# Kernel tuning notes

Hardware: AMD Instinct MI355X
Metric: run time of the kernel (lower is better)

The kernel has to match this reference:

```python
import jax, jax.numpy as jnp
import numpy as np
from math import factorial

R_MAX = 3.5
BASIS = 20
NORM2MOM_SILU = 1.679177  # e3nn normalize2mom constant for silu

# ---------- Wigner 3j (e3nn convention: real basis, Frobenius norm 1) ----------

def _su2_cg(j1, m1, j2, m2, j3, m3):
    if m3 != m1 + m2:
        return 0.0
    vmin = int(max(-j1 + j2 + m3, -j1 + m1, 0))
    vmax = int(min(j2 + j3 + m1, j3 - j1 + j2, j3 + m3))
    f = lambda n: factorial(round(n))
    C = ((2 * j3 + 1) * f(j3 + j1 - j2) * f(j3 - j1 + j2) * f(j1 + j2 - j3)
         * f(j3 + m3) * f(j3 - m3)
         / (f(j1 + j2 + j3 + 1) * f(j1 - m1) * f(j1 + m1) * f(j2 - m2) * f(j2 + m2))) ** 0.5
    S = 0.0
    for v in range(vmin, vmax + 1):
        S += (-1.0) ** (v + j2 + m2) / f(v) * f(j2 + j3 + m1 - v) * f(j1 - m1 + v) \
             / f(j3 - j1 + j2 - v) / f(j3 + m3 - v) / f(v + j1 - j2 - m3)
    return C * S


def _real_basis(l):
    q = np.zeros((2 * l + 1, 2 * l + 1), dtype=np.complex128)
    for m in range(-l, 0):
        q[l + m, l + abs(m)] = 2 ** -0.5
        q[l + m, l - abs(m)] = -1j * 2 ** -0.5
    q[l, l] = 1.0
    for m in range(1, l + 1):
        q[l + m, l + abs(m)] = (-1) ** m * 2 ** -0.5
        q[l + m, l - abs(m)] = 1j * (-1) ** m * 2 ** -0.5
    return (-1j) ** l * q


def wigner_3j(l1, l2, l3):
    C = np.zeros((2 * l1 + 1, 2 * l2 + 1, 2 * l3 + 1))
    for m1 in range(-l1, l1 + 1):
        for m2 in range(-l2, l2 + 1):
            if abs(m1 + m2) <= l3:
                C[l1 + m1, l2 + m2, l3 + m1 + m2] = _su2_cg(l1, m1, l2, m2, l3, m1 + m2)
    Q1, Q2, Q3 = _real_basis(l1), _real_basis(l2), _real_basis(l3)
    Cr = np.einsum('ij,kl,mn,ikn->jlm', Q1, Q2, np.conj(Q3.T), C.astype(np.complex128))
    assert np.abs(Cr.imag).max() < 1e-4
    Cr = Cr.real
    return (Cr / np.linalg.norm(Cr)).astype(np.float32)

# tp2 paths: (l1 from middle, l2 from sh) -> 2e (even parity, triangle inequality)
TP2_PATHS = [(0, 2), (1, 1), (1, 3), (2, 0), (2, 2), (3, 1), (3, 3)]
W3J = {p: jnp.asarray(wigner_3j(p[0], p[1], 2)) for p in TP2_PATHS}
ALPHA2 = (5.0 / 35.0) ** 0.5  # component norm: sqrt(dim(2e) / fan_in), fan_in = 7 paths * mul 5

# ---------- spherical harmonics, lmax=3, component normalization (e3nn axis convention) ----------

def spherical_harmonics(v):  # v: [E,3] unit vectors -> [E,16]
    x, y, z = v[:, 0], v[:, 1], v[:, 2]
    x2, y2, z2 = x * x, y * y, z * z
    s3, s5, s15 = 3.0 ** 0.5, 5.0 ** 0.5, 15.0 ** 0.5
    s70_4, s105, s42_4 = 70.0 ** 0.5 / 4, 105.0 ** 0.5, 42.0 ** 0.5 / 4
    s7_2, s105_2 = 7.0 ** 0.5 / 2, 105.0 ** 0.5 / 2
    sh = [jnp.ones_like(x),
          s3 * x, s3 * y, s3 * z,
          s15 * x * z, s15 * x * y, s5 * (y2 - 0.5 * (x2 + z2)), s15 * y * z, 0.5 * s15 * (z2 - x2),
          s70_4 * x * (3 * z2 - x2), s105 * x * y * z, s42_4 * x * (5 * y2 - 1.0),
          s7_2 * y * (5 * y2 - 3.0), s42_4 * z * (5 * y2 - 1.0), s105_2 * y * (z2 - x2),
          s70_4 * z * (z2 - 3 * x2)]
    return jnp.stack(sh, axis=-1)


def soft_one_hot(d):  # smooth_finite basis with cutoff on [0, R_MAX]
    values = jnp.linspace(0.0, R_MAX, BASIS + 2)[1:-1]
    step = R_MAX / (BASIS + 1)
    diff = (d[:, None] - values) / step
    def u(t):
        ts = jnp.where(t > 0, t, 1.0)
        return jnp.where(t > 0, jnp.exp(-1.0 / ts), 0.0)
    return 1.14136 * np.e ** 2 * u(diff + 1.0) * u(1.0 - diff)


def setup_inputs() -> dict:
    key = jax.random.key(0)
    ks = jax.random.split(key, 7)
    N, E = 50000, 600000
    edge_from = jax.random.randint(ks[2], (E,), 0, N)
    # no self-loops (avoids zero-length edge vectors, as radius_graph would)
    edge_to = (edge_from + jax.random.randint(ks[3], (E,), 1, N)) % N
    return {
        'x': jax.random.normal(ks[0], (N, 1), jnp.float32),
        'pos': jax.random.normal(ks[1], (N, 3), jnp.float32),
        'edge_from': edge_from,
        'edge_to': edge_to,
        'W1': jax.random.normal(ks[4], (20, 30), jnp.float32),
        'W2': jax.random.normal(ks[5], (30, 20), jnp.float32),
        'tp2_w': jax.random.normal(ks[6], (7, 5), jnp.float32),
    }


def reference(x, pos, edge_from, edge_to, W1, W2, tp2_w):
    E = edge_from.shape[0]
    N = x.shape[0]
    num_neighbors = 6.0
    edge_vec = pos[edge_to] - pos[edge_from]                 # [E,3]
    dist = jnp.linalg.norm(edge_vec, axis=1)                 # [E]
    sh = spherical_harmonics(edge_vec / dist[:, None])       # [E,16]
    emb = soft_one_hot(dist)                                 # [E,20]
    # FullyConnectedNet([20,30,20], silu) with e3nn normalization
    h = NORM2MOM_SILU * jax.nn.silu(emb @ W1 / jnp.sqrt(20.0))
    tp_w = (h @ W2 / jnp.sqrt(30.0)).reshape(E, 4, 5)        # per-edge tp1 weights
    s = x[edge_to, 0]                                        # [E] gathered 0e scalars
    sh_blocks = [sh[:, 0:1], sh[:, 1:4], sh[:, 4:9], sh[:, 9:16]]
    # tp1: 0e x l -> l ; alpha * w3j(0,l,l) collapses to identity per l
    mid = jnp.concatenate([
        (s[:, None, None] * tp_w[:, l, :, None] * sh_blocks[l][:, None, :]).reshape(E, 5 * (2 * l + 1))
        for l in range(4)], axis=-1)                         # [E,80]
    node_mid = jax.ops.segment_sum(mid, edge_from, num_segments=N) / jnp.sqrt(num_neighbors)
    m = node_mid[edge_to]                                    # [E,80]
    offs = [0, 5, 20, 45, 80]
    mid_blocks = [m[:, offs[l]:offs[l + 1]].reshape(E, 5, 2 * l + 1) for l in range(4)]
    out_e = jnp.zeros((E, 5), dtype=x.dtype)
    for p, (l1, l2) in enumerate(TP2_PATHS):
        out_e = out_e + ALPHA2 * jnp.einsum('ijk,eui,ej,u->ek', W3J[(l1, l2)],
                                            mid_blocks[l1], sh_blocks[l2], tp2_w[p])
    node_out = jax.ops.segment_sum(out_e, edge_from, num_segments=N) / jnp.sqrt(num_neighbors)
    Co = jnp.argmax(jnp.bincount(edge_to, length=N))         # torch.mode -> most frequent target node
    return node_out[Co]                                      # [5] = 1x2e
```

## Files before the change

kernel.cpp:

```cpp
#include <hip/hip_runtime.h>
#include <cmath>
#include <complex>
#include <algorithm>

#define NBH   16
#define CAP_S 512
#define CAP_T 64
#define CAP_M 4096
#define EB    64
#define HW_MAX 12544
#define BM_MAX 1568

namespace w3jhost {
static double fact(int n){
  static const double f[13]={1,1,2,6,24,120,720,5040,40320,362880,3628800,39916800,479001600};
  return f[n];
}
static double su2_cg(int j1,int m1,int j2,int m2,int j3,int m3){
  if(m3!=m1+m2) return 0.0;
  int vmin = std::max(std::max(-j1+j2+m3,-j1+m1),0);
  int vmax = std::min(std::min(j2+j3+m1, j3-j1+j2), j3+m3);
  double C = std::sqrt((double)(2*j3+1)*fact(j3+j1-j2)*fact(j3-j1+j2)*fact(j1+j2-j3)*fact(j3+m3)*fact(j3-m3)
            /(fact(j1+j2+j3+1)*fact(j1-m1)*fact(j1+m1)*fact(j2-m2)*fact(j2+m2)));
  double S=0.0;
  for(int v=vmin;v<=vmax;v++){
    double sgn = ((v+j2+m2)&1)?-1.0:1.0;
    S += sgn/fact(v)*fact(j2+j3+m1-v)*fact(j1-m1+v)/fact(j3-j1+j2-v)/fact(j3+m3-v)/fact(v+j1-j2-m3);
  }
  return C*S;
}
static void real_basis(int l, std::complex<double> q[7][7]){
  for(int i=0;i<7;i++)for(int j=0;j<7;j++) q[i][j]=0.0;
  const double r = std::sqrt(0.5);
  for(int m=-l;m<0;m++){ q[l+m][l-m]=r; q[l+m][l+m]=std::complex<double>(0.0,-r); }
  q[l][l]=1.0;
  for(int m=1;m<=l;m++){ double sg=(m&1)?-1.0:1.0; q[l+m][l+m]=sg*r; q[l+m][l-m]=std::complex<double>(0.0,sg*r); }
  std::complex<double> f;
  switch(l&3){ case 0: f={1,0};break; case 1: f={0,-1};break; case 2: f={-1,0};break; default: f={0,1};break; }
  for(int i=0;i<7;i++)for(int j=0;j<7;j++) q[i][j]*=f;
}
}

struct W3JArg { float w[675]; };

static W3JArg compute_w3j(){
  using namespace w3jhost;
  W3JArg out{};
  const int pl1[7]={0,1,1,2,2,3,3}, pl2[7]={2,1,3,0,2,1,3};
  int off=0;
  for(int p=0;p<7;p++){
    int l1=pl1[p], l2=pl2[p], l3=2;
    int n1=2*l1+1, n2=2*l2+1, n3=2*l3+1;
    double C[7][7][5];
    for(int i=0;i<7;i++)for(int k=0;k<7;k++)for(int n=0;n<5;n++) C[i][k][n]=0.0;
    for(int m1=-l1;m1<=l1;m1++)for(int m2=-l2;m2<=l2;m2++)
      if(std::abs(m1+m2)<=l3) C[l1+m1][l2+m2][l3+m1+m2]=su2_cg(l1,m1,l2,m2,l3,m1+m2);
    std::complex<double> Q1[7][7],Q2[7][7],Q3[7][7];
    real_basis(l1,Q1); real_basis(l2,Q2); real_basis(l3,Q3);
    double Cr[7][7][5]; double nrm=0.0;
    for(int a=0;a<n1;a++)for(int b=0;b<n2;b++)for(int c=0;c<n3;c++){
      std::complex<double> s(0.0,0.0);
      for(int i=0;i<n1;i++)for(int k=0;k<n2;k++)for(int n=0;n<n3;n++){
        double cv=C[i][k][n]; if(cv==0.0) continue;
        s += Q1[i][a]*Q2[k][b]*std::conj(Q3[n][c])*cv;
      }
      Cr[a][b][c]=s.real(); nrm+=s.real()*s.real();
    }
    nrm=std::sqrt(nrm);
    for(int a=0;a<n1;a++)for(int b=0;b<n2;b++)for(int c=0;c<n3;c++)
      out.w[off+(a*n2+b)*n3+c]=(float)(Cr[a][b][c]/nrm);
    off+=n1*n2*n3;
  }
  return out;
}
static const W3JArg g_w3j = compute_w3j();

__device__ __forceinline__ void calc_sh(float x,float y,float z,float* sh){
  float x2=x*x,y2=y*y,z2=z*z;
  const float s3=1.7320508075688772f, s5=2.2360679774997896f, s15=3.872983346207417f;
  const float s70_4=2.091650066335189f, s105=10.246950765959598f, s42_4=1.6201851746019651f;
  const float s7_2=1.3228756555322954f, s105_2=5.123475382979799f;
  sh[0]=1.f;
  sh[1]=s3*x; sh[2]=s3*y; sh[3]=s3*z;
  sh[4]=s15*x*z; sh[5]=s15*x*y; sh[6]=s5*(y2-0.5f*(x2+z2)); sh[7]=s15*y*z; sh[8]=0.5f*s15*(z2-x2);
  sh[9]=s70_4*x*(3.f*z2-x2); sh[10]=s105*x*y*z; sh[11]=s42_4*x*(5.f*y2-1.f);
  sh[12]=s7_2*y*(5.f*y2-3.f); sh[13]=s42_4*z*(5.f*y2-1.f); sh[14]=s105_2*y*(z2-x2); sh[15]=s70_4*z*(z2-3.f*x2);
}

__global__ void __launch_bounds__(1024,1)
k_hist(const int* __restrict__ eto, int E, int N, int* __restrict__ histg){
  __shared__ int hist[HW_MAX];
  const int HW=(N+3)>>2;
  const int tid=threadIdx.x;
  for(int w=tid;w<HW;w+=1024) hist[w]=0;
  __syncthreads();
  int nQ=(E+3)>>2;
  for(int q=blockIdx.x*1024+tid;q<nQ;q+=NBH*1024){
    int e=q*4;
    if(e+3<E){
      int4 v=*reinterpret_cast<const int4*>(eto+e);
      atomicAdd(&hist[v.x>>2], 1<<((v.x&3)*8));
      atomicAdd(&hist[v.y>>2], 1<<((v.y&3)*8));
      atomicAdd(&hist[v.z>>2], 1<<((v.z&3)*8));
      atomicAdd(&hist[v.w>>2], 1<<((v.w&3)*8));
    } else {
      for(;e<E;e++){ int t=eto[e]; atomicAdd(&hist[t>>2], 1<<((t&3)*8)); }
    }
  }
  __syncthreads();
  for(int w=tid;w<HW;w+=1024) histg[blockIdx.x*HW+w]=hist[w];
}

__global__ void __launch_bounds__(256,1)
k_argmax(const int* __restrict__ histg, int N, unsigned long long* __restrict__ packed){
  const int HW=(N+3)>>2;
  int w=blockIdx.x*256+threadIdx.x;
  unsigned long long lm=0ull;
  if(w<HW){
    int c0=0,c1=0,c2=0,c3=0;
    #pragma unroll
    for(int b=0;b<NBH;b++){
      int h=histg[b*HW+w];
      c0+=h&255; c1+=(h>>8)&255; c2+=(h>>16)&255; c3+=(int)((unsigned)h>>24);
    }
    int node=w*4;
    if(c0>0)          lm=max(lm,(((unsigned long long)(unsigned)c0)<<32)|(unsigned long long)(0xFFFFFFFFu-(unsigned)(node  )));
    if(node+1<N&&c1>0)lm=max(lm,(((unsigned long long)(unsigned)c1)<<32)|(unsigned long long)(0xFFFFFFFFu-(unsigned)(node+1)));
    if(node+2<N&&c2>0)lm=max(lm,(((unsigned long long)(unsigned)c2)<<32)|(unsigned long long)(0xFFFFFFFFu-(unsigned)(node+2)));
    if(node+3<N&&c3>0)lm=max(lm,(((unsigned long long)(unsigned)c3)<<32)|(unsigned long long)(0xFFFFFFFFu-(unsigned)(node+3)));
  }
  #pragma unroll
  for(int off=32;off;off>>=1){
    unsigned long long o=__shfl_xor(lm,off);
    lm=max(lm,o);
  }
  if((threadIdx.x&63)==0 && lm) atomicMax(packed,lm);
}

__global__ void __launch_bounds__(256,1)
k_collect(const int* __restrict__ efrom, int E,
          const unsigned long long* __restrict__ packed,
          int* __restrict__ S, int* __restrict__ numS){
  int co=(int)(0xFFFFFFFFu-(unsigned)((*packed)&0xFFFFFFFFull));
  int q=blockIdx.x*256+threadIdx.x;
  int e=q*4;
  if(e+3<E){
    int4 v=*reinterpret_cast<const int4*>(efrom+e);
    int f[4]={v.x,v.y,v.z,v.w};
    #pragma unroll
    for(int k=0;k<4;k++){
      if(f[k]==co){
        int p=atomicAdd(numS,1);
        if(p<CAP_S) S[p]=e+k;
      }
    }
  } else {
    for(;e<E;e++){
      if(efrom[e]==co){
        int p=atomicAdd(numS,1);
        if(p<CAP_S) S[p]=e;
      }
    }
  }
}

__global__ void __launch_bounds__(256,1)
k_scanM(const int* __restrict__ efrom, const int* __restrict__ eto, int E, int N,
        const int* __restrict__ S, const int* __restrict__ numS,
        int* __restrict__ M, int* __restrict__ numM){
  __shared__ int bitmap[BM_MAX];
  __shared__ int Te[CAP_T];
  __shared__ int Tlist[CAP_T];
  __shared__ int nTs;
  const int tid=threadIdx.x;
  int ns=*numS; if(ns>CAP_S) ns=CAP_S;
  int nsc=min(ns,CAP_T);
  const int BMW=(N+31)>>5;
  for(int w=tid;w<BMW;w+=256) bitmap[w]=0;
  if(tid<nsc) Te[tid]=eto[S[tid]];
  __syncthreads();
  if(tid<64){
    bool keep=false; int myv=0;
    if(tid<nsc){
      myv=Te[tid];
      keep=true;
      for(int k=0;k<tid;k++) if(Te[k]==myv){ keep=false; break; }
    }
    unsigned long long mask=__ballot(keep);
    if(keep){
      int slot=__popcll(mask&((1ull<<tid)-1ull));
      Tlist[slot]=myv;
    }
    if(tid==0) nTs=__popcll(mask);
  }
  __syncthreads();
  int nT=nTs;
  if(tid<nT){ int v=Tlist[tid]; atomicOr(&bitmap[v>>5], 1<<(v&31)); }
  __syncthreads();
  int q=blockIdx.x*256+tid;
  int e=q*4;
  if(e+3<E){
    int4 v=*reinterpret_cast<const int4*>(efrom+e);
    int f[4]={v.x,v.y,v.z,v.w};
    #pragma unroll
    for(int k=0;k<4;k++){
      int s=f[k];
      if((bitmap[s>>5]>>(s&31))&1){
        int sl=0;
        for(int kk=0;kk<nT;kk++) if(Tlist[kk]==s){ sl=kk; break; }
        int p=atomicAdd(numM,1);
        if(p<CAP_M) M[p]=(e+k)|(sl<<20);
      }
    }
  } else {
    for(;e<E;e++){
      int s=efrom[e];
      if((bitmap[s>>5]>>(s&31))&1){
        int sl=0;
        for(int kk=0;kk<nT;kk++) if(Tlist[kk]==s){ sl=kk; break; }
        int p=atomicAdd(numM,1);
        if(p<CAP_M) M[p]=e|(sl<<20);
      }
    }
  }
}

__global__ void __launch_bounds__(1024,1)
k_mlp(const float* __restrict__ x, const float* __restrict__ pos,
      const int* __restrict__ efrom, const int* __restrict__ eto,
      const float* __restrict__ W1, const float* __restrict__ W2,
      const int* __restrict__ M, const int* __restrict__ numM,
      float* __restrict__ nmid_g){
  __shared__ float W1s[600], W2s[600];
  __shared__ float shs[EB*16], embs[EB*20], hs[EB*30], tws[EB*20];
  __shared__ float es_[EB], dd_[EB];
  __shared__ int   sl_[EB];
  const int tid=threadIdx.x;
  int nm=*numM; if(nm>CAP_M) nm=CAP_M;
  for(int i=tid;i<600;i+=1024){ W1s[i]=W1[i]; W2s[i]=W2[i]; }
  int nb=(int)gridDim.x;
  int per=(nm+nb-1)/nb;
  int lo=min(nm,(int)blockIdx.x*per), hi=min(nm,lo+per);
  for(int base=lo;base<hi;base+=EB){
    int cnt=min(EB,hi-base);
    __syncthreads();
    if(tid<cnt){
      int m=M[base+tid];
      int e=m&0xFFFFF, sl=m>>20;
      sl_[tid]=sl;
      int a=efrom[e], b=eto[e];
      float dx=pos[3*b]-pos[3*a], dy=pos[3*b+1]-pos[3*a+1], dz=pos[3*b+2]-pos[3*a+2];
      float d=sqrtf(dx*dx+dy*dy+dz*dz);
      float inv=1.f/d;
      calc_sh(dx*inv,dy*inv,dz*inv,&shs[tid*16]);
      dd_[tid]=d;
      es_[tid]=x[b]*(0.18257418583505536f*0.4082482904638631f);
    }
    __syncthreads();
    for(int t=tid;t<cnt*20;t+=1024){
      int ee=t/20, i=t-ee*20;
      const float inv_step=21.f/3.5f;
      const float pref=(float)(1.14136*7.3890560989306495);
      float di=dd_[ee]*inv_step;
      float A=di-(float)i, B=(float)(i+2)-di;
      float ua=(A>0.f)?expf(-1.f/A):0.f;
      float ub=(B>0.f)?expf(-1.f/B):0.f;
      embs[ee*20+i]=pref*ua*ub;
    }
    __syncthreads();
    for(int t=tid;t<cnt*30;t+=1024){
      int ee=t/30, j=t-ee*30;
      float z=0.f;
      #pragma unroll
      for(int i=0;i<20;i++) z+=embs[ee*20+i]*W1s[i*30+j];
      z*=0.22360679774997896f;
      hs[ee*30+j]=1.679177f*z/(1.f+expf(-z));
    }
    __syncthreads();
    for(int t=tid;t<cnt*20;t+=1024){
      int ee=t/20, c=t-ee*20;
      float v=0.f;
      #pragma unroll
      for(int j=0;j<30;j++) v+=hs[ee*30+j]*W2s[j*20+c];
      tws[ee*20+c]=v;
    }
    __syncthreads();
    for(int t=tid;t<cnt*80;t+=1024){
      int ee=t/80, oo=t-ee*80;
      int sl=sl_[ee];
      int l,u,mm;
      if(oo<5){ l=0; u=oo; mm=0; }
      else if(oo<20){ int r=oo-5;  l=1; u=r/3; mm=r-u*3; }
      else if(oo<45){ int r=oo-20; l=2; u=r/5; mm=r-u*5; }
      else          { int r=oo-45; l=3; u=r/7; mm=r-u*7; }
      float val=es_[ee]*tws[ee*20+l*5+u]*shs[ee*16+l*l+mm];
      atomicAdd(&nmid_g[sl*80+oo],val);
    }
  }
}

__global__ void __launch_bounds__(1024,1)
k_final(const float* __restrict__ pos, const int* __restrict__ efrom, const int* __restrict__ eto,
        const float* __restrict__ tp2, const int* __restrict__ S, const int* __restrict__ numS,
        const float* __restrict__ nmid_g, W3JArg w3, float* __restrict__ out5){
  __shared__ float w3s[675];
  __shared__ float nmid_s[CAP_T*80];
  __shared__ float shs[EB*16];
  __shared__ float tp2s[35];
  __shared__ float acc[5];
  __shared__ int   Te[CAP_T], Tlist[CAP_T], sl_[EB], nTs;
  const int tid=threadIdx.x;
  for(int i=tid;i<675;i+=1024) w3s[i]=w3.w[i];
  if(tid<35) tp2s[tid]=tp2[tid];
  if(tid<5) acc[tid]=0.f;
  int ns=*numS; if(ns>CAP_S) ns=CAP_S;
  int nsc=min(ns,CAP_T);
  if(tid<nsc) Te[tid]=eto[S[tid]];
  __syncthreads();
  if(tid<64){
    bool keep=false; int myv=0;
    if(tid<nsc){
      myv=Te[tid];
      keep=true;
      for(int k=0;k<tid;k++) if(Te[k]==myv){ keep=false; break; }
    }
    unsigned long long mask=__ballot(keep);
    if(keep){
      int slot=__popcll(mask&((1ull<<tid)-1ull));
      Tlist[slot]=myv;
    }
    if(tid==0) nTs=__popcll(mask);
  }
  __syncthreads();
  int nT=nTs;
  for(int i=tid;i<nT*80;i+=1024) nmid_s[i]=nmid_g[i];
  for(int base=0;base<ns;base+=EB){
    int cnt=min(EB,ns-base);
    __syncthreads();
    if(tid<cnt){
      int e=S[base+tid];
      int a=efrom[e], b=eto[e];
      int sl=-1;
      for(int k=0;k<nT;k++) if(Tlist[k]==b){ sl=k; break; }
      sl_[tid]=sl;
      if(sl>=0){
        float dx=pos[3*b]-pos[3*a], dy=pos[3*b+1]-pos[3*a+1], dz=pos[3*b+2]-pos[3*a+2];
        float d=sqrtf(dx*dx+dy*dy+dz*dz);
        float inv=1.f/d;
        calc_sh(dx*inv,dy*inv,dz*inv,&shs[tid*16]);
      }
    }
    __syncthreads();
    for(int t=tid;t<cnt*35;t+=1024){
      int ee=t/35, r=t-ee*35, p=r/5, u=r-p*5;
      int sl=sl_[ee];
      if(sl>=0){
        int l1=(p+1)>>1;
        int l2=(0x3636>>(2*p))&3;
        const unsigned long long wbpack=
          (25ULL<<9)|(70ULL<<18)|(175ULL<<27)|(200ULL<<36)|(325ULL<<45)|(430ULL<<54);
        int wb=(int)((wbpack>>(9*p))&511ULL);
        int n1=2*l1+1, n2=2*l2+1;
        float tu=tp2s[p*5+u];
        float o0=0.f,o1=0.f,o2=0.f,o3=0.f,o4=0.f;
        const float* mrow=&nmid_s[sl*80+5*l1*l1+u*n1];
        const float* shrow=&shs[ee*16+l2*l2];
        const float* Wp=&w3s[wb];
        for(int i=0;i<n1;i++){
          float mi=mrow[i]*tu;
          for(int j=0;j<n2;j++){
            float c=mi*shrow[j];
            const float* Wk=Wp+(i*n2+j)*5;
            o0+=Wk[0]*c; o1+=Wk[1]*c; o2+=Wk[2]*c; o3+=Wk[3]*c; o4+=Wk[4]*c;
          }
        }
        atomicAdd(&acc[0],o0); atomicAdd(&acc[1],o1); atomicAdd(&acc[2],o2);
        atomicAdd(&acc[3],o3); atomicAdd(&acc[4],o4);
      }
    }
    __syncthreads();
  }
  __syncthreads();
  const float scale=0.37796447300922725f*0.4082482904638631f;
  if(tid<5) out5[tid]=acc[tid]*scale;
}

extern "C" void kernel_launch(void* const* d_in, const int* in_sizes, int n_in,
                              void* d_out, int out_size, void* d_ws, size_t ws_size,
                              hipStream_t stream){
  const float* x    =(const float*)d_in[0];
  const float* pos  =(const float*)d_in[1];
  const int*   efrom=(const int*)  d_in[2];
  const int*   eto  =(const int*)  d_in[3];
  const float* W1   =(const float*)d_in[4];
  const float* W2   =(const float*)d_in[5];
  const float* tp2  =(const float*)d_in[6];
  int N=in_sizes[0], E=in_sizes[2];
  int HW=(N+3)>>2;

  char* ws=(char*)d_ws;
  size_t o=0;
  unsigned long long* packed=(unsigned long long*)(ws+o); o+=8;
  int* numS=(int*)(ws+o);                   o+=4;
  int* numM=(int*)(ws+o);                   o+=4;
  o=(o+63)&~(size_t)63;
  float* nmid_g=(float*)(ws+o);             o+=(size_t)CAP_T*80*4;
  size_t zlen=o;
  int* histg=(int*)(ws+o);                  o+=(size_t)NBH*HW*4;
  int* S=(int*)(ws+o);                      o+=(size_t)CAP_S*4;
  int* M=(int*)(ws+o);                      o+=(size_t)CAP_M*4;

  (void)hipMemsetAsync(d_ws,0,zlen,stream);

  int nQ=(E+3)>>2;
  int gScan=(nQ+255)/256;
  int gArg =(HW+255)/256;
  k_hist   <<<NBH,1024,0,stream>>>(eto,E,N,histg);
  k_argmax <<<gArg,256,0,stream>>>(histg,N,packed);
  k_collect<<<gScan,256,0,stream>>>(efrom,E,packed,S,numS);
  k_scanM  <<<gScan,256,0,stream>>>(efrom,eto,E,N,S,numS,M,numM);
  k_mlp    <<<16,1024,0,stream>>>(x,pos,efrom,eto,W1,W2,M,numM,nmid_g);
  k_final  <<<1,1024,0,stream>>>(pos,efrom,eto,tp2,S,numS,nmid_g,g_w3j,(float*)d_out);
}
```

Measured before the change: 114.2 us.

## Fuse six kernels into two persistent kernels with software grid barriers

Merges the histogram, argmax, source-edge collection and neighbour scan into one persistent 64-block kernel, and the MLP and final tensor-product stages into one 16-block kernel. The stages are separated by atomic-counter grid barriers instead of kernel launches. The histogram is also spread over 64 blocks instead of 16, and nmid zeroing moves into the kernel, which shrinks the memset. This removes per-launch overhead and launch gaps. In exchange it relies on all blocks being co-resident for the spin barriers, and the argmax stage must now read 64 partial histograms.

```diff
diff --git a/kernel.cpp b/kernel.cpp
--- a/kernel.cpp
+++ b/kernel.cpp
@@ -3,7 +3,9 @@
 #include <complex>
 #include <algorithm>
 
-#define NBH   16
+#define NB1   64
+#define TB    1024
+#define NB2   16
 #define CAP_S 512
 #define CAP_T 64
 #define CAP_M 4096
@@ -87,160 +89,187 @@
   sh[12]=s7_2*y*(5.f*y2-3.f); sh[13]=s42_4*z*(5.f*y2-1.f); sh[14]=s105_2*y*(z2-x2); sh[15]=s70_4*z*(z2-3.f*x2);
 }
 
-__global__ void __launch_bounds__(1024,1)
-k_hist(const int* __restrict__ eto, int E, int N, int* __restrict__ histg){
-  __shared__ int hist[HW_MAX];
+__device__ __forceinline__ void cstore(int* p,int v){ __hip_atomic_store(p,v,__ATOMIC_RELAXED,__HIP_MEMORY_SCOPE_AGENT); }
+__device__ __forceinline__ int  cload(const int* p){ return __hip_atomic_load(p,__ATOMIC_RELAXED,__HIP_MEMORY_SCOPE_AGENT); }
+__device__ __forceinline__ void cstoref(float* p,float v){ __hip_atomic_store(p,v,__ATOMIC_RELAXED,__HIP_MEMORY_SCOPE_AGENT); }
+__device__ __forceinline__ float cloadf(const float* p){ return __hip_atomic_load(p,__ATOMIC_RELAXED,__HIP_MEMORY_SCOPE_AGENT); }
+
+__device__ __forceinline__ void gridbar(int* ctr,int count){
+  __syncthreads();
+  if(threadIdx.x==0){
+    asm volatile("s_waitcnt vmcnt(0) lgkmcnt(0)" ::: "memory");
+    __hip_atomic_fetch_add(ctr,1,__ATOMIC_RELAXED,__HIP_MEMORY_SCOPE_AGENT);
+    int it=0;
+    while(__hip_atomic_load(ctr,__ATOMIC_RELAXED,__HIP_MEMORY_SCOPE_AGENT)<count){
+      if(it<16) __builtin_amdgcn_s_sleep(2);
+      else      __builtin_amdgcn_s_sleep(16);
+      ++it;
+    }
+  }
+  __syncthreads();
+}
+
+__global__ void __launch_bounds__(TB,1)
+k_front(const int* __restrict__ eto, const int* __restrict__ efrom, int E, int N,
+        int* __restrict__ histg, unsigned long long* __restrict__ packed,
+        int* __restrict__ numS, int* __restrict__ S,
+        int* __restrict__ numM, int* __restrict__ M,
+        float* __restrict__ nmid_g, int* __restrict__ bars){
+  __shared__ union LdsU {
+    int hist[HW_MAX];
+    struct { int bitmap[BM_MAX]; int Te[CAP_T]; int Tlist[CAP_T]; } s;
+  } U;
+  __shared__ int nTs;
+  const int tid=threadIdx.x, bid=blockIdx.x;
+  const int gtid=bid*TB+tid, gstride=NB1*TB;
   const int HW=(N+3)>>2;
-  const int tid=threadIdx.x;
-  for(int w=tid;w<HW;w+=1024) hist[w]=0;
-  __syncthreads();
-  int nQ=(E+3)>>2;
-  for(int q=blockIdx.x*1024+tid;q<nQ;q+=NBH*1024){
+  const int nQ=(E+3)>>2;
+
+  for(int i=gtid;i<CAP_T*80;i+=gstride) cstoref(&nmid_g[i],0.f);
+  for(int w=tid;w<HW;w+=TB) U.hist[w]=0;
+  __syncthreads();
+  for(int q=gtid;q<nQ;q+=gstride){
     int e=q*4;
     if(e+3<E){
       int4 v=*reinterpret_cast<const int4*>(eto+e);
-      atomicAdd(&hist[v.x>>2], 1<<((v.x&3)*8));
-      atomicAdd(&hist[v.y>>2], 1<<((v.y&3)*8));
-      atomicAdd(&hist[v.z>>2], 1<<((v.z&3)*8));
-      atomicAdd(&hist[v.w>>2], 1<<((v.w&3)*8));
+      atomicAdd(&U.hist[v.x>>2], 1<<((v.x&3)*8));
+      atomicAdd(&U.hist[v.y>>2], 1<<((v.y&3)*8));
+      atomicAdd(&U.hist[v.z>>2], 1<<((v.z&3)*8));
+      atomicAdd(&U.hist[v.w>>2], 1<<((v.w&3)*8));
     } else {
-      for(;e<E;e++){ int t=eto[e]; atomicAdd(&hist[t>>2], 1<<((t&3)*8)); }
-    }
-  }
-  __syncthreads();
-  for(int w=tid;w<HW;w+=1024) histg[blockIdx.x*HW+w]=hist[w];
-}
-
-__global__ void __launch_bounds__(256,1)
-k_argmax(const int* __restrict__ histg, int N, unsigned long long* __restrict__ packed){
-  const int HW=(N+3)>>2;
-  int w=blockIdx.x*256+threadIdx.x;
-  unsigned long long lm=0ull;
-  if(w<HW){
-    int c0=0,c1=0,c2=0,c3=0;
+      for(;e<E;e++){ int t=eto[e]; atomicAdd(&U.hist[t>>2], 1<<((t&3)*8)); }
+    }
+  }
+  __syncthreads();
+  for(int w=tid;w<HW;w+=TB) cstore(&histg[bid*HW+w],U.hist[w]);
+  gridbar(&bars[0],NB1);
+
+  {
+    unsigned long long lm=0ull;
+    for(int w=gtid;w<HW;w+=gstride){
+      int c0=0,c1=0,c2=0,c3=0;
+      for(int b=0;b<NB1;b++){
+        int h=cload(&histg[b*HW+w]);
+        c0+=h&255; c1+=(h>>8)&255; c2+=(h>>16)&255; c3+=(int)((unsigned)h>>24);
+      }
+      int node=w*4;
+      if(c0>0)           lm=max(lm,(((unsigned long long)(unsigned)c0)<<32)|(unsigned long long)(0xFFFFFFFFu-(unsigned)(node  )));
+      if(node+1<N&&c1>0) lm=max(lm,(((unsigned long long)(unsigned)c1)<<32)|(unsigned long long)(0xFFFFFFFFu-(unsigned)(node+1)));
+      if(node+2<N&&c2>0) lm=max(lm,(((unsigned long long)(unsigned)c2)<<32)|(unsigned long long)(0xFFFFFFFFu-(unsigned)(node+2)));
+      if(node+3<N&&c3>0) lm=max(lm,(((unsigned long long)(unsigned)c3)<<32)|(unsigned long long)(0xFFFFFFFFu-(unsigned)(node+3)));
+    }
     #pragma unroll
-    for(int b=0;b<NBH;b++){
-      int h=histg[b*HW+w];
-      c0+=h&255; c1+=(h>>8)&255; c2+=(h>>16)&255; c3+=(int)((unsigned)h>>24);
-    }
-    int node=w*4;
-    if(c0>0)          lm=max(lm,(((unsigned long long)(unsigned)c0)<<32)|(unsigned long long)(0xFFFFFFFFu-(unsigned)(node  )));
-    if(node+1<N&&c1>0)lm=max(lm,(((unsigned long long)(unsigned)c1)<<32)|(unsigned long long)(0xFFFFFFFFu-(unsigned)(node+1)));
-    if(node+2<N&&c2>0)lm=max(lm,(((unsigned long long)(unsigned)c2)<<32)|(unsigned long long)(0xFFFFFFFFu-(unsigned)(node+2)));
-    if(node+3<N&&c3>0)lm=max(lm,(((unsigned long long)(unsigned)c3)<<32)|(unsigned long long)(0xFFFFFFFFu-(unsigned)(node+3)));
-  }
-  #pragma unroll
-  for(int off=32;off;off>>=1){
-    unsigned long long o=__shfl_xor(lm,off);
-    lm=max(lm,o);
-  }
-  if((threadIdx.x&63)==0 && lm) atomicMax(packed,lm);
-}
-
-__global__ void __launch_bounds__(256,1)
-k_collect(const int* __restrict__ efrom, int E,
-          const unsigned long long* __restrict__ packed,
-          int* __restrict__ S, int* __restrict__ numS){
-  int co=(int)(0xFFFFFFFFu-(unsigned)((*packed)&0xFFFFFFFFull));
-  int q=blockIdx.x*256+threadIdx.x;
-  int e=q*4;
-  if(e+3<E){
-    int4 v=*reinterpret_cast<const int4*>(efrom+e);
-    int f[4]={v.x,v.y,v.z,v.w};
-    #pragma unroll
-    for(int k=0;k<4;k++){
-      if(f[k]==co){
-        int p=atomicAdd(numS,1);
-        if(p<CAP_S) S[p]=e+k;
-      }
-    }
-  } else {
-    for(;e<E;e++){
-      if(efrom[e]==co){
-        int p=atomicAdd(numS,1);
-        if(p<CAP_S) S[p]=e;
-      }
-    }
-  }
-}
-
-__global__ void __launch_bounds__(256,1)
-k_scanM(const int* __restrict__ efrom, const int* __restrict__ eto, int E, int N,
-        const int* __restrict__ S, const int* __restrict__ numS,
-        int* __restrict__ M, int* __restrict__ numM){
-  __shared__ int bitmap[BM_MAX];
-  __shared__ int Te[CAP_T];
-  __shared__ int Tlist[CAP_T];
-  __shared__ int nTs;
-  const int tid=threadIdx.x;
-  int ns=*numS; if(ns>CAP_S) ns=CAP_S;
-  int nsc=min(ns,CAP_T);
-  const int BMW=(N+31)>>5;
-  for(int w=tid;w<BMW;w+=256) bitmap[w]=0;
-  if(tid<nsc) Te[tid]=eto[S[tid]];
-  __syncthreads();
-  if(tid<64){
-    bool keep=false; int myv=0;
-    if(tid<nsc){
-      myv=Te[tid];
-      keep=true;
-      for(int k=0;k<tid;k++) if(Te[k]==myv){ keep=false; break; }
-    }
-    unsigned long long mask=__ballot(keep);
-    if(keep){
-      int slot=__popcll(mask&((1ull<<tid)-1ull));
-      Tlist[slot]=myv;
-    }
-    if(tid==0) nTs=__popcll(mask);
-  }
-  __syncthreads();
-  int nT=nTs;
-  if(tid<nT){ int v=Tlist[tid]; atomicOr(&bitmap[v>>5], 1<<(v&31)); }
-  __syncthreads();
-  int q=blockIdx.x*256+tid;
-  int e=q*4;
-  if(e+3<E){
-    int4 v=*reinterpret_cast<const int4*>(efrom+e);
-    int f[4]={v.x,v.y,v.z,v.w};
-    #pragma unroll
-    for(int k=0;k<4;k++){
-      int s=f[k];
-      if((bitmap[s>>5]>>(s&31))&1){
-        int sl=0;
-        for(int kk=0;kk<nT;kk++) if(Tlist[kk]==s){ sl=kk; break; }
-        int p=atomicAdd(numM,1);
-        if(p<CAP_M) M[p]=(e+k)|(sl<<20);
-      }
-    }
-  } else {
-    for(;e<E;e++){
-      int s=efrom[e];
-      if((bitmap[s>>5]>>(s&31))&1){
-        int sl=0;
-        for(int kk=0;kk<nT;kk++) if(Tlist[kk]==s){ sl=kk; break; }
-        int p=atomicAdd(numM,1);
-        if(p<CAP_M) M[p]=e|(sl<<20);
-      }
-    }
-  }
-}
-
-__global__ void __launch_bounds__(1024,1)
-k_mlp(const float* __restrict__ x, const float* __restrict__ pos,
-      const int* __restrict__ efrom, const int* __restrict__ eto,
-      const float* __restrict__ W1, const float* __restrict__ W2,
-      const int* __restrict__ M, const int* __restrict__ numM,
-      float* __restrict__ nmid_g){
+    for(int off=32;off;off>>=1){
+      unsigned long long o=__shfl_xor(lm,off);
+      lm=max(lm,o);
+    }
+    if((tid&63)==0 && lm) atomicMax(packed,lm);
+  }
+  gridbar(&bars[1],NB1);
+
+  {
+    unsigned long long pk=__hip_atomic_load(packed,__ATOMIC_RELAXED,__HIP_MEMORY_SCOPE_AGENT);
+    int co=(int)(0xFFFFFFFFu-(unsigned)(pk&0xFFFFFFFFull));
+    for(int q=gtid;q<nQ;q+=gstride){
+      int e=q*4;
+      if(e+3<E){
+        int4 v=*reinterpret_cast<const int4*>(efrom+e);
+        int f[4]={v.x,v.y,v.z,v.w};
+        #pragma unroll
+        for(int k=0;k<4;k++){
+          if(f[k]==co){
+            int p=atomicAdd(numS,1);
+            if(p<CAP_S) cstore(&S[p],e+k);
+          }
+        }
+      } else {
+        for(;e<E;e++){
+          if(efrom[e]==co){
+            int p=atomicAdd(numS,1);
+            if(p<CAP_S) cstore(&S[p],e);
+          }
+        }
+      }
+    }
+  }
+  gridbar(&bars[2],NB1);
+
+  {
+    int ns=cload(numS); if(ns>CAP_S) ns=CAP_S;
+    int nsc=min(ns,CAP_T);
+    const int BMW=(N+31)>>5;
+    for(int w=tid;w<BMW;w+=TB) U.s.bitmap[w]=0;
+    if(tid<nsc) U.s.Te[tid]=eto[cload(&S[tid])];
+    __syncthreads();
+    if(tid<64){
+      bool keep=false; int myv=0;
+      if(tid<nsc){
+        myv=U.s.Te[tid];
+        keep=true;
+        for(int k=0;k<tid;k++) if(U.s.Te[k]==myv){ keep=false; break; }
+      }
+      unsigned long long mask=__ballot(keep);
+      if(keep){
+        int slot=__popcll(mask&((1ull<<tid)-1ull));
+        U.s.Tlist[slot]=myv;
+      }
+      if(tid==0) nTs=__popcll(mask);
+    }
+    __syncthreads();
+    int nT=nTs;
+    if(tid<nT){ int v=U.s.Tlist[tid]; atomicOr(&U.s.bitmap[v>>5], 1<<(v&31)); }
+    __syncthreads();
+    for(int q=gtid;q<nQ;q+=gstride){
+      int e=q*4;
+      if(e+3<E){
+        int4 v=*reinterpret_cast<const int4*>(efrom+e);
+        int f[4]={v.x,v.y,v.z,v.w};
+        #pragma unroll
+        for(int k=0;k<4;k++){
+          int s=f[k];
+          if((U.s.bitmap[s>>5]>>(s&31))&1){
+            int sl=0;
+            for(int kk=0;kk<nT;kk++) if(U.s.Tlist[kk]==s){ sl=kk; break; }
+            int p=atomicAdd(numM,1);
+            if(p<CAP_M) cstore(&M[p],(e+k)|(sl<<20));
+          }
+        }
+      } else {
+        for(;e<E;e++){
+          int s=efrom[e];
+          if((U.s.bitmap[s>>5]>>(s&31))&1){
+            int sl=0;
+            for(int kk=0;kk<nT;kk++) if(U.s.Tlist[kk]==s){ sl=kk; break; }
+            int p=atomicAdd(numM,1);
+            if(p<CAP_M) cstore(&M[p],e|(sl<<20));
+          }
+        }
+      }
+    }
+  }
+}
+
+__global__ void __launch_bounds__(TB,1)
+k_tail(const float* __restrict__ x, const float* __restrict__ pos,
+       const int* __restrict__ efrom, const int* __restrict__ eto,
+       const float* __restrict__ W1, const float* __restrict__ W2,
+       const float* __restrict__ tp2,
+       const int* __restrict__ S, const int* __restrict__ numS,
+       const int* __restrict__ M, const int* __restrict__ numM,
+       float* __restrict__ nmid_g, int* __restrict__ bars,
+       W3JArg w3, float* __restrict__ out5){
   __shared__ float W1s[600], W2s[600];
   __shared__ float shs[EB*16], embs[EB*20], hs[EB*30], tws[EB*20];
   __shared__ float es_[EB], dd_[EB];
   __shared__ int   sl_[EB];
-  const int tid=threadIdx.x;
+  __shared__ float w3s[675], nmid_s[CAP_T*80], tp2s[35], acc[5];
+  __shared__ int   Te[CAP_T], Tlist[CAP_T], nTs;
+  const int tid=threadIdx.x, bid=blockIdx.x;
+
   int nm=*numM; if(nm>CAP_M) nm=CAP_M;
-  for(int i=tid;i<600;i+=1024){ W1s[i]=W1[i]; W2s[i]=W2[i]; }
-  int nb=(int)gridDim.x;
-  int per=(nm+nb-1)/nb;
-  int lo=min(nm,(int)blockIdx.x*per), hi=min(nm,lo+per);
+  for(int i=tid;i<600;i+=TB){ W1s[i]=W1[i]; W2s[i]=W2[i]; }
+  int per=(nm+NB2-1)/NB2;
+  int lo=min(nm,bid*per), hi=min(nm,lo+per);
   for(int base=lo;base<hi;base+=EB){
     int cnt=min(EB,hi-base);
     __syncthreads();
@@ -257,7 +286,7 @@
       es_[tid]=x[b]*(0.18257418583505536f*0.4082482904638631f);
     }
     __syncthreads();
-    for(int t=tid;t<cnt*20;t+=1024){
+    for(int t=tid;t<cnt*20;t+=TB){
       int ee=t/20, i=t-ee*20;
       const float inv_step=21.f/3.5f;
       const float pref=(float)(1.14136*7.3890560989306495);
@@ -268,7 +297,7 @@
       embs[ee*20+i]=pref*ua*ub;
     }
     __syncthreads();
-    for(int t=tid;t<cnt*30;t+=1024){
+    for(int t=tid;t<cnt*30;t+=TB){
       int ee=t/30, j=t-ee*30;
       float z=0.f;
       #pragma unroll
@@ -277,7 +306,7 @@
       hs[ee*30+j]=1.679177f*z/(1.f+expf(-z));
     }
     __syncthreads();
-    for(int t=tid;t<cnt*20;t+=1024){
+    for(int t=tid;t<cnt*20;t+=TB){
       int ee=t/20, c=t-ee*20;
       float v=0.f;
       #pragma unroll
@@ -285,7 +314,7 @@
       tws[ee*20+c]=v;
     }
     __syncthreads();
-    for(int t=tid;t<cnt*80;t+=1024){
+    for(int t=tid;t<cnt*80;t+=TB){
       int ee=t/80, oo=t-ee*80;
       int sl=sl_[ee];
       int l,u,mm;
@@ -297,20 +326,10 @@
       atomicAdd(&nmid_g[sl*80+oo],val);
     }
   }
-}
-
-__global__ void __launch_bounds__(1024,1)
-k_final(const float* __restrict__ pos, const int* __restrict__ efrom, const int* __restrict__ eto,
-        const float* __restrict__ tp2, const int* __restrict__ S, const int* __restrict__ numS,
-        const float* __restrict__ nmid_g, W3JArg w3, float* __restrict__ out5){
-  __shared__ float w3s[675];
-  __shared__ float nmid_s[CAP_T*80];
-  __shared__ float shs[EB*16];
-  __shared__ float tp2s[35];
-  __shared__ float acc[5];
-  __shared__ int   Te[CAP_T], Tlist[CAP_T], sl_[EB], nTs;
-  const int tid=threadIdx.x;
-  for(int i=tid;i<675;i+=1024) w3s[i]=w3.w[i];
+  gridbar(&bars[3],NB2);
+  if(bid!=0) return;
+
+  for(int i=tid;i<675;i+=TB) w3s[i]=w3.w[i];
   if(tid<35) tp2s[tid]=tp2[tid];
   if(tid<5) acc[tid]=0.f;
   int ns=*numS; if(ns>CAP_S) ns=CAP_S;
@@ -333,7 +352,7 @@
   }
   __syncthreads();
   int nT=nTs;
-  for(int i=tid;i<nT*80;i+=1024) nmid_s[i]=nmid_g[i];
+  for(int i=tid;i<nT*80;i+=TB) nmid_s[i]=cloadf(&nmid_g[i]);
   for(int base=0;base<ns;base+=EB){
     int cnt=min(EB,ns-base);
     __syncthreads();
@@ -351,7 +370,7 @@
       }
     }
     __syncthreads();
-    for(int t=tid;t<cnt*35;t+=1024){
+    for(int t=tid;t<cnt*35;t+=TB){
       int ee=t/35, r=t-ee*35, p=r/5, u=r-p*5;
       int sl=sl_[ee];
       if(sl>=0){
@@ -403,22 +422,16 @@
   unsigned long long* packed=(unsigned long long*)(ws+o); o+=8;
   int* numS=(int*)(ws+o);                   o+=4;
   int* numM=(int*)(ws+o);                   o+=4;
+  int* bars=(int*)(ws+o);                   o+=8*4;
+  size_t ctrl=o;
   o=(o+63)&~(size_t)63;
-  float* nmid_g=(float*)(ws+o);             o+=(size_t)CAP_T*80*4;
-  size_t zlen=o;
-  int* histg=(int*)(ws+o);                  o+=(size_t)NBH*HW*4;
+  int* histg=(int*)(ws+o);                  o+=(size_t)NB1*HW*4;
   int* S=(int*)(ws+o);                      o+=(size_t)CAP_S*4;
   int* M=(int*)(ws+o);                      o+=(size_t)CAP_M*4;
-
-  (void)hipMemsetAsync(d_ws,0,zlen,stream);
-
-  int nQ=(E+3)>>2;
-  int gScan=(nQ+255)/256;
-  int gArg =(HW+255)/256;
-  k_hist   <<<NBH,1024,0,stream>>>(eto,E,N,histg);
-  k_argmax <<<gArg,256,0,stream>>>(histg,N,packed);
-  k_collect<<<gScan,256,0,stream>>>(efrom,E,packed,S,numS);
-  k_scanM  <<<gScan,256,0,stream>>>(efrom,eto,E,N,S,numS,M,numM);
-  k_mlp    <<<16,1024,0,stream>>>(x,pos,efrom,eto,W1,W2,M,numM,nmid_g);
-  k_final  <<<1,1024,0,stream>>>(pos,efrom,eto,tp2,S,numS,nmid_g,g_w3j,(float*)d_out);
-}
+  float* nmid_g=(float*)(ws+o);             o+=(size_t)CAP_T*80*4;
+
+  (void)hipMemsetAsync(d_ws,0,ctrl,stream);
+
+  k_front<<<NB1,TB,0,stream>>>(eto,efrom,E,N,histg,packed,numS,S,numM,M,nmid_g,bars);
+  k_tail <<<NB2,TB,0,stream>>>(x,pos,efrom,eto,W1,W2,tp2,S,numS,M,numM,nmid_g,bars,g_w3j,(float*)d_out);
+}
```

After: 126.4 us. 10.7% more time.

## Fuse MLP and final kernels with grid barrier and drop workspace memset

Applied to the files above, without the earlier changes.

The MLP scatter kernel and the single-block final contraction are merged into one 16-block kernel. A spin-wait grid barrier on an atomic counter separates them, and block 0 then finishes the contraction, reading the node accumulators with relaxed agent-scope atomic loads. The host memset is removed: the histogram kernel now zeroes the control words and the accumulator buffer, and that kernel's block count is doubled. This saves one kernel launch and the memset, at the cost of relying on all 16 blocks being resident at once and on a hand-written barrier for memory ordering.

```diff
diff --git a/kernel.cpp b/kernel.cpp
--- a/kernel.cpp
+++ b/kernel.cpp
@@ -3,7 +3,8 @@
 #include <complex>
 #include <algorithm>
 
-#define NBH   16
+#define NBH   32
+#define NB2   16
 #define CAP_S 512
 #define CAP_T 64
 #define CAP_M 4096
@@ -87,11 +88,32 @@
   sh[12]=s7_2*y*(5.f*y2-3.f); sh[13]=s42_4*z*(5.f*y2-1.f); sh[14]=s105_2*y*(z2-x2); sh[15]=s70_4*z*(z2-3.f*x2);
 }
 
+__device__ __forceinline__ float cloadf(const float* p){ return __hip_atomic_load(p,__ATOMIC_RELAXED,__HIP_MEMORY_SCOPE_AGENT); }
+
+__device__ __forceinline__ void gridbar(int* ctr,int count){
+  __syncthreads();
+  if(threadIdx.x==0){
+    asm volatile("s_waitcnt vmcnt(0) lgkmcnt(0)" ::: "memory");
+    __hip_atomic_fetch_add(ctr,1,__ATOMIC_RELAXED,__HIP_MEMORY_SCOPE_AGENT);
+    int it=0;
+    while(__hip_atomic_load(ctr,__ATOMIC_RELAXED,__HIP_MEMORY_SCOPE_AGENT)<count){
+      if(it<16) __builtin_amdgcn_s_sleep(2);
+      else      __builtin_amdgcn_s_sleep(16);
+      ++it;
+    }
+  }
+  __syncthreads();
+}
+
 __global__ void __launch_bounds__(1024,1)
-k_hist(const int* __restrict__ eto, int E, int N, int* __restrict__ histg){
+k_hist(const int* __restrict__ eto, int E, int N, int* __restrict__ histg,
+       int* __restrict__ ctrl ,
+       float* __restrict__ nmid_g){
   __shared__ int hist[HW_MAX];
   const int HW=(N+3)>>2;
   const int tid=threadIdx.x;
+  if(blockIdx.x==0 && tid<12) ctrl[tid]=0;
+  for(int i=blockIdx.x*1024+tid;i<CAP_T*80;i+=NBH*1024) nmid_g[i]=0.f;
   for(int w=tid;w<HW;w+=1024) hist[w]=0;
   __syncthreads();
   int nQ=(E+3)>>2;
@@ -226,21 +248,26 @@
 }
 
 __global__ void __launch_bounds__(1024,1)
-k_mlp(const float* __restrict__ x, const float* __restrict__ pos,
-      const int* __restrict__ efrom, const int* __restrict__ eto,
-      const float* __restrict__ W1, const float* __restrict__ W2,
-      const int* __restrict__ M, const int* __restrict__ numM,
-      float* __restrict__ nmid_g){
+k_tail(const float* __restrict__ x, const float* __restrict__ pos,
+       const int* __restrict__ efrom, const int* __restrict__ eto,
+       const float* __restrict__ W1, const float* __restrict__ W2,
+       const float* __restrict__ tp2,
+       const int* __restrict__ S, const int* __restrict__ numS,
+       const int* __restrict__ M, const int* __restrict__ numM,
+       float* __restrict__ nmid_g, int* __restrict__ bars,
+       W3JArg w3, float* __restrict__ out5){
   __shared__ float W1s[600], W2s[600];
   __shared__ float shs[EB*16], embs[EB*20], hs[EB*30], tws[EB*20];
   __shared__ float es_[EB], dd_[EB];
   __shared__ int   sl_[EB];
-  const int tid=threadIdx.x;
+  __shared__ float w3s[675], nmid_s[CAP_T*80], tp2s[35], acc[5];
+  __shared__ int   Te[CAP_T], Tlist[CAP_T], nTs;
+  const int tid=threadIdx.x, bid=blockIdx.x;
+
   int nm=*numM; if(nm>CAP_M) nm=CAP_M;
   for(int i=tid;i<600;i+=1024){ W1s[i]=W1[i]; W2s[i]=W2[i]; }
-  int nb=(int)gridDim.x;
-  int per=(nm+nb-1)/nb;
-  int lo=min(nm,(int)blockIdx.x*per), hi=min(nm,lo+per);
+  int per=(nm+NB2-1)/NB2;
+  int lo=min(nm,bid*per), hi=min(nm,lo+per);
   for(int base=lo;base<hi;base+=EB){
     int cnt=min(EB,hi-base);
     __syncthreads();
@@ -297,19 +324,9 @@
       atomicAdd(&nmid_g[sl*80+oo],val);
     }
   }
-}
-
-__global__ void __launch_bounds__(1024,1)
-k_final(const float* __restrict__ pos, const int* __restrict__ efrom, const int* __restrict__ eto,
-        const float* __restrict__ tp2, const int* __restrict__ S, const int* __restrict__ numS,
-        const float* __restrict__ nmid_g, W3JArg w3, float* __restrict__ out5){
-  __shared__ float w3s[675];
-  __shared__ float nmid_s[CAP_T*80];
-  __shared__ float shs[EB*16];
-  __shared__ float tp2s[35];
-  __shared__ float acc[5];
-  __shared__ int   Te[CAP_T], Tlist[CAP_T], sl_[EB], nTs;
-  const int tid=threadIdx.x;
+  gridbar(&bars[0],NB2);
+  if(bid!=0) return;
+
   for(int i=tid;i<675;i+=1024) w3s[i]=w3.w[i];
   if(tid<35) tp2s[tid]=tp2[tid];
   if(tid<5) acc[tid]=0.f;
@@ -333,7 +350,7 @@
   }
   __syncthreads();
   int nT=nTs;
-  for(int i=tid;i<nT*80;i+=1024) nmid_s[i]=nmid_g[i];
+  for(int i=tid;i<nT*80;i+=1024) nmid_s[i]=cloadf(&nmid_g[i]);
   for(int base=0;base<ns;base+=EB){
     int cnt=min(EB,ns-base);
     __syncthreads();
@@ -400,25 +417,23 @@
 
   char* ws=(char*)d_ws;
   size_t o=0;
+  int* ctrl=(int*)(ws+o);
   unsigned long long* packed=(unsigned long long*)(ws+o); o+=8;
   int* numS=(int*)(ws+o);                   o+=4;
   int* numM=(int*)(ws+o);                   o+=4;
+  int* bars=(int*)(ws+o);                   o+=8*4;
   o=(o+63)&~(size_t)63;
-  float* nmid_g=(float*)(ws+o);             o+=(size_t)CAP_T*80*4;
-  size_t zlen=o;
   int* histg=(int*)(ws+o);                  o+=(size_t)NBH*HW*4;
   int* S=(int*)(ws+o);                      o+=(size_t)CAP_S*4;
   int* M=(int*)(ws+o);                      o+=(size_t)CAP_M*4;
-
-  (void)hipMemsetAsync(d_ws,0,zlen,stream);
+  float* nmid_g=(float*)(ws+o);             o+=(size_t)CAP_T*80*4;
 
   int nQ=(E+3)>>2;
   int gScan=(nQ+255)/256;
   int gArg =(HW+255)/256;
-  k_hist   <<<NBH,1024,0,stream>>>(eto,E,N,histg);
+  k_hist   <<<NBH,1024,0,stream>>>(eto,E,N,histg,ctrl,nmid_g);
   k_argmax <<<gArg,256,0,stream>>>(histg,N,packed);
   k_collect<<<gScan,256,0,stream>>>(efrom,E,packed,S,numS);
   k_scanM  <<<gScan,256,0,stream>>>(efrom,eto,E,N,S,numS,M,numM);
-  k_mlp    <<<16,1024,0,stream>>>(x,pos,efrom,eto,W1,W2,M,numM,nmid_g);
-  k_final  <<<1,1024,0,stream>>>(pos,efrom,eto,tp2,S,numS,nmid_g,g_w3j,(float*)d_out);
-}
+  k_tail   <<<NB2,1024,0,stream>>>(x,pos,efrom,eto,W1,W2,tp2,S,numS,M,numM,nmid_g,bars,g_w3j,(float*)d_out);
+}
```

New measurement: 110.7 us, median of 2. 1.03x faster.
